# Performance work log

Measured on AMD Instinct MI355X. Metric: run time of the kernel, lower is better.

The kernel has to match this reference:

```python
import jax, jax.numpy as jnp
import numpy as np


def setup_inputs() -> dict:
    key = jax.random.key(0)
    k1, k2 = jax.random.split(key)
    B, t, nbands, framesize = 32, 4000, 65, 80
    H = jax.random.normal(k1, (B, t, nbands), dtype=jnp.float32)
    noise = jax.random.uniform(k2, (B, t, framesize), dtype=jnp.float32)  # uniform [0,1); scaled to [-1,1) in reference
    return {"H": H, "noise": noise, "framesize": framesize}


def reference(H, noise, framesize):
    # H: [B, t, nbands] real half-spectrum of zero-phase filter
    B, t, nbands = H.shape
    L_fir = 2 * nbands - 1  # FIR length (129)

    # zero-phase impulse response -> linear-phase via circular shift
    zero_phase = jnp.fft.irfft(H, n=L_fir, axis=-1)          # [B, t, L_fir]
    lin_phase = jnp.roll(zero_phase, nbands - 1, axis=-1)

    # periodic Hann window (matches torch.hann_window default periodic=True)
    n = jnp.arange(L_fir, dtype=H.dtype)
    hann = 0.5 * (1.0 - jnp.cos(2.0 * jnp.pi * n / L_fir))
    firwin = lin_phase * hann                                 # [B, t, L_fir]

    # per-frame noise in [-1, 1)
    x = noise * 2.0 - 1.0                                     # [B, t, framesize]

    # full FFT convolution along last axis
    L = framesize + L_fir - 1                                 # 208
    X = jnp.fft.rfft(x, n=L, axis=-1)
    W = jnp.fft.rfft(firwin, n=L, axis=-1)
    filtered = jnp.fft.irfft(X * W, n=L, axis=-1)             # [B, t, L]

    # overlap-add with hop = framesize via scatter-add (replaces conv_transpose1d trick)
    total = (t - 1) * framesize + L
    idx = jnp.arange(t)[:, None] * framesize + jnp.arange(L)[None, :]  # [t, L]
    out = jnp.zeros((B, total), dtype=filtered.dtype).at[:, idx].add(filtered)

    # trim filter group delay from both ends -> [B, t*framesize]
    return out[:, nbands - 1: total - (nbands - 1)]
```

## Files before the change

### kernel.cpp

```cpp
#include <hip/hip_runtime.h>


#define NT 256
#define X_STRIDE 84
#define W_STRIDE 158
#define W_P 18
#define NSLOT 35
#define WTOT_H 5544
#define HF_STRIDE 104
#define HTOT_H 4992
#define XTOT_H 2940

typedef _Float16 f16x8 __attribute__((ext_vector_type(8)));
typedef _Float16 f16x4 __attribute__((ext_vector_type(4)));
typedef _Float16 h2 __attribute__((ext_vector_type(2)));
typedef float f32x4 __attribute__((ext_vector_type(4)));

union U32H2 { unsigned u; h2 h; };
static __device__ __forceinline__ h2 mid_h2(h2 lo, h2 hi) {
  U32H2 a, b; a.h = lo; b.h = hi;
  U32H2 o; o.u = __builtin_amdgcn_alignbit(b.u, a.u, 16);
  return o.h;
}

__global__ void __launch_bounds__(256)
minit_kernel(_Float16* __restrict__ M) {
  const float TP = 6.28318530717958647692f / 129.f;
  int i = blockIdx.x * 256 + threadIdx.x;
  int frag = i >> 9;
  int off  = i & 511;
  int lane = off >> 3, j = off & 7;
  int nt = frag / 3, ks = frag - 3 * (frag / 3);
  int n = nt * 16 + (lane & 15);
  int k = ks * 32 + (lane >> 4) * 8 + j;
  float v = 0.f;
  if (n <= 128 && k <= 64) {
    float hann = 0.5f - 0.5f * __cosf((float)n * TP);
    float sc = (k == 0 ? 1.f : 2.f) * (1.f / 129.f);
    int e = (k * (n - 64)) % 129; if (e < 0) e += 129;
    v = hann * sc * __cosf((float)e * TP);
  }
  M[i] = (_Float16)v;
}

__global__ void __launch_bounds__(NT)
fng_kernel(const float* __restrict__ Hg_, const float* __restrict__ Ng_,
           float* __restrict__ Og_, const _Float16* __restrict__ Mg) {
  __shared__ __align__(16) _Float16 sWh[WTOT_H];
  __shared__ __align__(16) _Float16 sXh[XTOT_H];
  __shared__ __align__(16) _Float16 sHf[HTOT_H];

  const int t  = threadIdx.x;
  const int bx = blockIdx.x;
  const int b  = blockIdx.y;
  const int f0 = bx * 32;

  {
    float4 z4 = {0.f, 0.f, 0.f, 0.f};
    for (int i = t; i < WTOT_H / 8; i += NT) ((float4*)sWh)[i] = z4;
  }

  {
    const float* Hg = Hg_ + (size_t)b * (4000 * 65);
#pragma unroll
    for (int j = 0; j < 4; ++j) {
      int i = t + NT * j;
      if (i < 35 * 24) {
        int r = i / 24, u = i - 24 * r;
        int fr = f0 - 2 + r;
        f16x4 o = {(_Float16)0.f, (_Float16)0.f, (_Float16)0.f, (_Float16)0.f};
        if (u < 16) {
          if (fr >= 0 && fr < 4000) {
            const float* hp = &Hg[fr * 65 + 4 * u];
            o.x = (_Float16)hp[0]; o.y = (_Float16)hp[1];
            o.z = (_Float16)hp[2]; o.w = (_Float16)hp[3];
          }
          *(f16x4*)&sHf[r * HF_STRIDE + 4 * u] = o;
        } else if (u == 16) {
          if (fr >= 0 && fr < 4000) o.x = (_Float16)Hg[fr * 65 + 64];
          *(f16x4*)&sHf[r * HF_STRIDE + 64] = o;
        } else {
          *(f16x4*)&sHf[r * HF_STRIDE + 4 * u] = o;
        }
      }
    }
  }

  {
    const float* Ng = Ng_ + (size_t)b * 320000;
#pragma unroll
    for (int j = 0; j < 3; ++j) {
      int q = t + NT * j;
      if (q < NSLOT * 20) {
        int fi = q / 20, qm = q - 20 * fi;
        int fr = f0 - 2 + fi;
        f16x4 o = {(_Float16)0.f, (_Float16)0.f, (_Float16)0.f, (_Float16)0.f};
        if (fr >= 0 && fr < 4000) {
          float4 v = *(const float4*)&Ng[(size_t)fr * 80 + 4 * qm];
          o.x = (_Float16)(2.f * v.w - 1.f);
          o.y = (_Float16)(2.f * v.z - 1.f);
          o.z = (_Float16)(2.f * v.y - 1.f);
          o.w = (_Float16)(2.f * v.x - 1.f);
        }
        *(f16x4*)&sXh[fi * X_STRIDE + (76 - 4 * qm)] = o;
      }
    }
  }
  __syncthreads();

  {
    const int wv   = t >> 6;
    const int lane = t & 63;
    const int quad = lane >> 4;
    const int l15  = lane & 15;
#pragma unroll 1
    for (int tile = wv; tile < 27; tile += 4) {
      const int mt = tile / 9, nt = tile - 9 * (tile / 9);
      f32x4 acc = {0.f, 0.f, 0.f, 0.f};
#pragma unroll
      for (int ks = 0; ks < 3; ++ks) {
        f16x8 a = *(const f16x8*)&sHf[(mt * 16 + l15) * HF_STRIDE + ks * 32 + quad * 8];
        f16x8 bb = ((const f16x8*)Mg)[(nt * 3 + ks) * 64 + lane];
        acc = __builtin_amdgcn_mfma_f32_16x16x32_f16(a, bb, acc, 0, 0, 0);
      }
      const int n = nt * 16 + l15;
      const int fr0 = mt * 16 + quad * 4;
      if (n <= 128) {
#pragma unroll
        for (int r = 0; r < 4; ++r) {
          int frame = fr0 + r;
          if (frame < NSLOT) sWh[frame * W_STRIDE + W_P + n] = (_Float16)acc[r];
        }
      }
    }
  }
  __syncthreads();

  {
    const int col = t & 31;
    const int pb  = t >> 5;
    const int e   = 64 + 10 * pb;
    const int qq  = (e >= 80) ? 1 : 0;
    const int D   = e - 80 * qq;
    float acc[10];
#pragma unroll
    for (int i = 0; i < 10; ++i) acc[i] = 0.f;

#pragma unroll 1
    for (int g = 2; g >= -1; --g) {
      const int dlt = D + 80 * g;
      int Ulo = (dlt - 128) >> 3; if (Ulo < 0) Ulo = 0;
      int Uhi = (dlt + 9) >> 3;   if (Uhi > 9) Uhi = 9;
      if (Ulo > Uhi) continue;
      const int slot = col + qq - g + 2;
      const _Float16* wr = &sWh[slot * W_STRIDE];
      const _Float16* xr = &sXh[slot * X_STRIDE];
      int wb = W_P + dlt - 8 * Ulo - 4;

      h2 wEa[10], wOa[9];
#pragma unroll
      for (int k2 = 0; k2 < 10; ++k2) wEa[k2] = *(const h2*)&wr[wb - 4 + 2 * k2];
#pragma unroll
      for (int k2 = 0; k2 < 9; ++k2) wOa[k2] = mid_h2(wEa[k2], wEa[k2 + 1]);

#define PAIRX(K) (((K) & 1) ? wOa[(((K) - 1) >> 1) + 2] : wEa[(((K) >> 1) + 2)])
#pragma unroll 4
      for (int U = Ulo; U <= Uhi; ++U) {
        const _Float16* xp = &xr[72 - 8 * U];
        f16x4 q0 = *(const f16x4*)&xp[0];
        f16x4 q1 = *(const f16x4*)&xp[4];
        h2 xD; xD.x = q0.x; xD.y = q0.y;
        h2 xC; xC.x = q0.z; xC.y = q0.w;
        h2 xB; xB.x = q1.x; xB.y = q1.y;
        h2 xA; xA.x = q1.z; xA.y = q1.w;
#pragma unroll
        for (int i = 0; i < 10; ++i) {
          float a = acc[i];
          a = __builtin_amdgcn_fdot2(xA, PAIRX(i + 3), a, false);
          a = __builtin_amdgcn_fdot2(xB, PAIRX(i + 1), a, false);
          a = __builtin_amdgcn_fdot2(xC, PAIRX(i - 1), a, false);
          a = __builtin_amdgcn_fdot2(xD, PAIRX(i - 3), a, false);
          acc[i] = a;
        }
        int wl = wb - 12; if (wl < 0) wl = 0;
        const _Float16* wp = &wr[wl];
#pragma unroll
        for (int k2 = 9; k2 >= 4; --k2) wEa[k2] = wEa[k2 - 4];
#pragma unroll
        for (int k2 = 8; k2 >= 4; --k2) wOa[k2] = wOa[k2 - 4];
        wEa[0] = *(const h2*)&wp[0];
        wEa[1] = *(const h2*)&wp[2];
        wEa[2] = *(const h2*)&wp[4];
        wEa[3] = *(const h2*)&wp[6];
        wOa[0] = mid_h2(wEa[0], wEa[1]);
        wOa[1] = mid_h2(wEa[1], wEa[2]);
        wOa[2] = mid_h2(wEa[2], wEa[3]);
        wOa[3] = mid_h2(wEa[3], wEa[4]);
        wb -= 8;
      }
#undef PAIRX
    }

    float* Ob = Og_ + (size_t)b * 320000 + 2560 * bx + 80 * col + 10 * pb;
#pragma unroll
    for (int s = 0; s < 5; ++s) {
      float2 v; v.x = acc[2 * s]; v.y = acc[2 * s + 1];
      *(float2*)&Ob[2 * s] = v;
    }
  }
}

extern "C" void kernel_launch(void* const* d_in, const int* in_sizes, int n_in,
                              void* d_out, int out_size, void* d_ws, size_t ws_size,
                              hipStream_t stream) {
  const float* H     = (const float*)d_in[0];
  const float* noise = (const float*)d_in[1];
  float* out = (float*)d_out;
  _Float16* M = (_Float16*)d_ws;
  (void)in_sizes; (void)n_in; (void)ws_size; (void)out_size;

  minit_kernel<<<54, 256, 0, stream>>>(M);
  dim3 grid(125, 32, 1);
  fng_kernel<<<grid, NT, 0, stream>>>(H, noise, out, M);
}
```

Baseline: 168.2 us.

## Load H directly into MFMA registers and drop shared H staging

Removes the shared-memory staging buffer for H: each of three waves loads its 16 frames of H straight from global into f16 MFMA operand registers and sweeps all nine N-tiles, instead of tiles being spread across four waves reading from LDS. It also zeroes only the padding regions of the W buffer, drops a syncthreads, widens the left padding so the clamp on the W pointer can be removed, and sets launch bounds to 8 blocks per CU. The aim is less LDS traffic, a smaller LDS footprint and higher occupancy. In exchange the fourth wave sits idle during the GEMM, and H is read from global with per-lane strided loads.

Result: faster. 153.8 us (-8.6%).

```diff
diff --git a/kernel.cpp b/kernel.cpp
--- a/kernel.cpp
+++ b/kernel.cpp
@@ -3,12 +3,10 @@
 
 #define NT 256
 #define X_STRIDE 84
-#define W_STRIDE 158
-#define W_P 18
+#define W_STRIDE 154
+#define W_P 24
 #define NSLOT 35
-#define WTOT_H 5544
-#define HF_STRIDE 104
-#define HTOT_H 4992
+#define WTOT_H 5416
 #define XTOT_H 2940
 
 typedef _Float16 f16x8 __attribute__((ext_vector_type(8)));
@@ -43,12 +41,11 @@
   M[i] = (_Float16)v;
 }
 
-__global__ void __launch_bounds__(NT)
+__global__ void __launch_bounds__(NT, 8)
 fng_kernel(const float* __restrict__ Hg_, const float* __restrict__ Ng_,
            float* __restrict__ Og_, const _Float16* __restrict__ Mg) {
   __shared__ __align__(16) _Float16 sWh[WTOT_H];
   __shared__ __align__(16) _Float16 sXh[XTOT_H];
-  __shared__ __align__(16) _Float16 sHf[HTOT_H];
 
   const int t  = threadIdx.x;
   const int bx = blockIdx.x;
@@ -56,32 +53,15 @@
   const int f0 = bx * 32;
 
   {
-    float4 z4 = {0.f, 0.f, 0.f, 0.f};
-    for (int i = t; i < WTOT_H / 8; i += NT) ((float4*)sWh)[i] = z4;
-  }
-
-  {
-    const float* Hg = Hg_ + (size_t)b * (4000 * 65);
-#pragma unroll
-    for (int j = 0; j < 4; ++j) {
-      int i = t + NT * j;
-      if (i < 35 * 24) {
-        int r = i / 24, u = i - 24 * r;
-        int fr = f0 - 2 + r;
-        f16x4 o = {(_Float16)0.f, (_Float16)0.f, (_Float16)0.f, (_Float16)0.f};
-        if (u < 16) {
-          if (fr >= 0 && fr < 4000) {
-            const float* hp = &Hg[fr * 65 + 4 * u];
-            o.x = (_Float16)hp[0]; o.y = (_Float16)hp[1];
-            o.z = (_Float16)hp[2]; o.w = (_Float16)hp[3];
-          }
-          *(f16x4*)&sHf[r * HF_STRIDE + 4 * u] = o;
-        } else if (u == 16) {
-          if (fr >= 0 && fr < 4000) o.x = (_Float16)Hg[fr * 65 + 64];
-          *(f16x4*)&sHf[r * HF_STRIDE + 64] = o;
-        } else {
-          *(f16x4*)&sHf[r * HF_STRIDE + 4 * u] = o;
-        }
+#pragma unroll
+    for (int it = 0; it < 4; ++it) {
+      int j = t + NT * it;
+      if (j < 24) {
+        sWh[j] = (_Float16)0.f;
+      } else if (j < 899) {
+        int jj = j - 24;
+        int c = jj / 25, o = jj - 25 * c;
+        sWh[c * W_STRIDE + 153 + o] = (_Float16)0.f;
       }
     }
   }
@@ -106,30 +86,54 @@
       }
     }
   }
-  __syncthreads();
 
   {
     const int wv   = t >> 6;
     const int lane = t & 63;
-    const int quad = lane >> 4;
-    const int l15  = lane & 15;
-#pragma unroll 1
-    for (int tile = wv; tile < 27; tile += 4) {
-      const int mt = tile / 9, nt = tile - 9 * (tile / 9);
-      f32x4 acc = {0.f, 0.f, 0.f, 0.f};
-#pragma unroll
-      for (int ks = 0; ks < 3; ++ks) {
-        f16x8 a = *(const f16x8*)&sHf[(mt * 16 + l15) * HF_STRIDE + ks * 32 + quad * 8];
-        f16x8 bb = ((const f16x8*)Mg)[(nt * 3 + ks) * 64 + lane];
-        acc = __builtin_amdgcn_mfma_f32_16x16x32_f16(a, bb, acc, 0, 0, 0);
-      }
-      const int n = nt * 16 + l15;
-      const int fr0 = mt * 16 + quad * 4;
-      if (n <= 128) {
-#pragma unroll
-        for (int r = 0; r < 4; ++r) {
-          int frame = fr0 + r;
-          if (frame < NSLOT) sWh[frame * W_STRIDE + W_P + n] = (_Float16)acc[r];
+    if (wv < 3) {
+      const int quad = lane >> 4;
+      const int l15  = lane & 15;
+      const int mt   = wv;
+      const int fr   = f0 - 2 + mt * 16 + l15;
+      const bool va  = (fr >= 0 && fr < 4000);
+      const int frc  = va ? fr : 0;
+      const float* hr = Hg_ + (size_t)b * 260000 + (size_t)frc * 65;
+
+      float c0[8], c1[8];
+      __builtin_memcpy(c0, &hr[quad * 8], 32);
+      __builtin_memcpy(c1, &hr[32 + quad * 8], 32);
+      float s64 = hr[64];
+      if (!va) {
+#pragma unroll
+        for (int j = 0; j < 8; ++j) { c0[j] = 0.f; c1[j] = 0.f; }
+        s64 = 0.f;
+      }
+      f16x8 a0, a1, a2;
+#pragma unroll
+      for (int j = 0; j < 8; ++j) {
+        a0[j] = (_Float16)c0[j];
+        a1[j] = (_Float16)c1[j];
+        a2[j] = (_Float16)0.f;
+      }
+      if (quad == 0) a2[0] = (_Float16)s64;
+
+#pragma unroll 3
+      for (int nt = 0; nt < 9; ++nt) {
+        f32x4 acc = {0.f, 0.f, 0.f, 0.f};
+        f16x8 b0 = ((const f16x8*)Mg)[(nt * 3 + 0) * 64 + lane];
+        f16x8 b1 = ((const f16x8*)Mg)[(nt * 3 + 1) * 64 + lane];
+        f16x8 b2 = ((const f16x8*)Mg)[(nt * 3 + 2) * 64 + lane];
+        acc = __builtin_amdgcn_mfma_f32_16x16x32_f16(a0, b0, acc, 0, 0, 0);
+        acc = __builtin_amdgcn_mfma_f32_16x16x32_f16(a1, b1, acc, 0, 0, 0);
+        acc = __builtin_amdgcn_mfma_f32_16x16x32_f16(a2, b2, acc, 0, 0, 0);
+        const int n = nt * 16 + l15;
+        if (n <= 128) {
+          const int fb = mt * 16 + quad * 4;
+#pragma unroll
+          for (int r = 0; r < 4; ++r) {
+            int frame = fb + r;
+            if (frame < NSLOT) sWh[frame * W_STRIDE + W_P + n] = (_Float16)acc[r];
+          }
         }
       }
     }
@@ -182,8 +186,7 @@
           a = __builtin_amdgcn_fdot2(xD, PAIRX(i - 3), a, false);
           acc[i] = a;
         }
-        int wl = wb - 12; if (wl < 0) wl = 0;
-        const _Float16* wp = &wr[wl];
+        const _Float16* wp = &wr[wb - 12];
 #pragma unroll
         for (int k2 = 9; k2 >= 4; --k2) wEa[k2] = wEa[k2 - 4];
 #pragma unroll
```
